# Performance work log

Measured on AMD Instinct MI355X. Metric: run time of the kernel, lower is better.

## Reference

```python
import jax, jax.numpy as jnp
import numpy as np

B, N, D, H = 4, 1024, 1024, 16
DK = D // H
NEG_INF = jnp.finfo(jnp.float32).min


def setup_inputs() -> dict:
    key = jax.random.key(0)
    ks = jax.random.split(key, 6)
    x = jax.random.normal(ks[0], (B, N, D), dtype=jnp.float32)
    # padding mask: True where padded; vary lengths per batch element
    lengths = jnp.array([N, N - 128, N - 256, N - 512], dtype=jnp.int32)
    mask = jnp.arange(N)[None, :] >= lengths[:, None]  # [B, N] bool
    s = (1.0 / np.sqrt(D)).astype(np.float32)  # xavier-ish scale
    Wq = jax.random.normal(ks[1], (D, D), dtype=jnp.float32) * s
    Wk = jax.random.normal(ks[2], (D, D), dtype=jnp.float32) * s
    Wv = jax.random.normal(ks[3], (D, D), dtype=jnp.float32) * s
    Wo = jax.random.normal(ks[4], (D, D), dtype=jnp.float32) * s
    z = jnp.zeros((D,), dtype=jnp.float32)
    return {"x": x, "mask": mask, "Wq": Wq, "bq": z, "Wk": Wk, "bk": z,
            "Wv": Wv, "bv": z, "Wo": Wo, "bo": z}


def reference(x, mask, Wq, bq, Wk, bk, Wv, bv, Wo, bo):
    b, n, d = x.shape
    scale = jnp.asarray(DK, x.dtype) ** -0.5
    # QKV projections (weights stored [out, in] like torch Linear)
    def proj(W, bias):
        y = jnp.einsum('bnd,ed->bne', x, W) + bias
        return y.reshape(b, n, H, DK).transpose(0, 2, 1, 3)  # [B,H,N,Dk]
    q = proj(Wq, bq)
    k = proj(Wk, bk)
    v = proj(Wv, bv)
    energy = jnp.einsum('bhqd,bhkd->bhqk', q, k) * scale  # [B,H,N,N]
    energy = jnp.where(mask[:, None, None, :], NEG_INF, energy)
    weights = jax.nn.softmax(energy, axis=-1)
    attn = jnp.einsum('bhqk,bhkd->bhqd', weights, v)  # [B,H,N,Dk]
    attn = attn.transpose(0, 2, 1, 3).reshape(b, n, d)
    return jnp.einsum('bnd,ed->bne', attn, Wo) + bo
```

## Files before the change

kernel.cpp:

```cpp
#include <hip/hip_runtime.h>

#define DEV __device__ __forceinline__

typedef __attribute__((ext_vector_type(8))) short s16x8;
typedef __attribute__((ext_vector_type(4))) float f32x4;
typedef __attribute__((ext_vector_type(4))) unsigned short u16x4;
typedef __attribute__((ext_vector_type(2))) unsigned int u32x2;

static constexpr int Bb = 4, Nn = 1024, Dd = 1024, Hh = 16, DKk = 64;

DEV unsigned short f2bf(float f) {
    union { float f; unsigned int u; } x; x.f = f;
    unsigned int r = x.u + 0x7FFFu + ((x.u >> 16) & 1u);
    return (unsigned short)(r >> 16);
}

DEV float fexp2(float x) {
#if __has_builtin(__builtin_amdgcn_exp2f)
    return __builtin_amdgcn_exp2f(x);
#else
    return exp2f(x);
#endif
}

DEV void gld16(const void* g, void* l) {
    __builtin_amdgcn_global_load_lds(
        (const __attribute__((address_space(1))) void*)g,
        (__attribute__((address_space(3))) void*)l, 16, 0, 0);
}

DEV void wait_vm4_barrier() {
    __builtin_amdgcn_sched_barrier(0);
    asm volatile("s_waitcnt vmcnt(4)" ::: "memory");
    __builtin_amdgcn_sched_barrier(0);
    __builtin_amdgcn_s_barrier();
}

__global__ __launch_bounds__(256) void cast_k(const float* __restrict__ x,
                                              const float* __restrict__ Wq,
                                              const float* __restrict__ Wk,
                                              const float* __restrict__ Wv,
                                              const float* __restrict__ Wo,
                                              const unsigned int* __restrict__ mraw,
                                              unsigned short* __restrict__ xb,
                                              unsigned short* __restrict__ Wqb,
                                              unsigned short* __restrict__ Wkb,
                                              unsigned short* __restrict__ Wvb,
                                              unsigned short* __restrict__ Wob,
                                              int* __restrict__ lengths) {
    if (blockIdx.x == 4096) {
        __shared__ int is_u8;
        const int tid = threadIdx.x;
        if (tid == 0) is_u8 = 0;
        __syncthreads();
        int nz = 0;
        for (int i = tid; i < 1024; i += 256) nz |= (mraw[i] != 0u) ? 1 : 0;
        if (nz) is_u8 = 1;
        __syncthreads();
        const int wv = tid >> 6, lane = tid & 63;
        int cnt = 0;
        if (is_u8) {
            const unsigned char* b8 = (const unsigned char*)mraw;
            for (int n = lane; n < Nn; n += 64) cnt += (b8[wv * Nn + n] == 0) ? 1 : 0;
        } else {
            for (int n = lane; n < Nn; n += 64) cnt += (mraw[wv * Nn + n] == 0u) ? 1 : 0;
        }
#pragma unroll
        for (int off = 32; off; off >>= 1) cnt += __shfl_xor(cnt, off);
        if (lane == 0) lengths[wv] = cnt;
        return;
    }
    const size_t i = ((size_t)blockIdx.x * 256 + threadIdx.x) * 8;
    const float* src;
    unsigned short* dst;
    size_t off;
    const size_t XE = (size_t)4 * 1024 * 1024, WE = (size_t)1024 * 1024;
    if (i < XE) {
        src = x; dst = xb; off = i;
    } else {
        size_t j = i - XE;
        int w = (int)(j >> 20);
        off = j & (WE - 1);
        src = (w == 0) ? Wq : (w == 1) ? Wk : (w == 2) ? Wv : Wo;
        dst = (w == 0) ? Wqb : (w == 1) ? Wkb : (w == 2) ? Wvb : Wob;
    }
    f32x4 a = *(const f32x4*)(src + off);
    f32x4 b = *(const f32x4*)(src + off + 4);
    s16x8 t;
    t[0] = (short)f2bf(a[0]); t[1] = (short)f2bf(a[1]);
    t[2] = (short)f2bf(a[2]); t[3] = (short)f2bf(a[3]);
    t[4] = (short)f2bf(b[0]); t[5] = (short)f2bf(b[1]);
    t[6] = (short)f2bf(b[2]); t[7] = (short)f2bf(b[3]);
    *(s16x8*)(dst + off) = t;
}

DEV void gemm_kloop(const unsigned short* __restrict__ A,
                    const unsigned short* __restrict__ W,
                    char* lA, char* lB, int bm, int bn,
                    int tid, int kstep0, f32x4 (&acc)[4][4]) {
    const int wv = tid >> 6, lane = tid & 63, g = lane >> 4, lr = lane & 15;
    const int wr = wv >> 1, wc = wv & 1;

    const int rbase = wv * 8 + (lane >> 3);
    const int corig = (lane & 7) ^ (lane >> 3);
    const unsigned short* Asrc = A + (size_t)(bm + rbase) * Dd + corig * 8;
    const unsigned short* Bsrc = W + (size_t)(bn + rbase) * Dd + corig * 8;
    const int ldsb = wv * 1024;
    const int xk = (lr & 7);

    int kstep = kstep0;
    for (int it = 0; it < 16; ++it) {
        const int k0 = kstep * 64;
#pragma unroll
        for (int p = 0; p < 4; ++p) {
            gld16(Asrc + (size_t)(p * 32) * Dd + k0, lA + p * 4096 + ldsb);
            gld16(Bsrc + (size_t)(p * 32) * Dd + k0, lB + p * 4096 + ldsb);
        }
        __syncthreads();
#pragma unroll
        for (int s = 0; s < 2; ++s) {
            s16x8 af[4], bf[4];
#pragma unroll
            for (int m = 0; m < 4; ++m)
                af[m] = *(const s16x8*)(lA + (wr * 64 + m * 16 + lr) * 128 + (((s * 4 + g) ^ xk) << 4));
#pragma unroll
            for (int n = 0; n < 4; ++n)
                bf[n] = *(const s16x8*)(lB + (wc * 64 + n * 16 + lr) * 128 + (((s * 4 + g) ^ xk) << 4));
#pragma unroll
            for (int m = 0; m < 4; ++m)
#pragma unroll
                for (int n = 0; n < 4; ++n)
                    acc[m][n] = __builtin_amdgcn_mfma_f32_16x16x32_bf16(af[m], bf[n], acc[m][n], 0, 0, 0);
        }
        __syncthreads();
        kstep = (kstep + 1) & 15;
    }
}

__global__ __launch_bounds__(256, 4) void gemm_qkv_k(const unsigned short* __restrict__ xb,
                                                     const unsigned short* __restrict__ Wqb,
                                                     const unsigned short* __restrict__ Wkb,
                                                     const unsigned short* __restrict__ Wvb,
                                                     const float* __restrict__ bq,
                                                     const float* __restrict__ bk,
                                                     const float* __restrict__ bv,
                                                     const int* __restrict__ lengths,
                                                     unsigned short* __restrict__ Qo,
                                                     unsigned short* __restrict__ Ko,
                                                     unsigned short* __restrict__ Vo) {
    __shared__ __align__(16) char lA[128 * 64 * 2];
    __shared__ __align__(16) char lB[128 * 64 * 2];
    const int z = blockIdx.z;
    const int bm = blockIdx.x * 128, bn = blockIdx.y * 128;
    if (z != 0 && (bm & 1023) >= lengths[bm >> 10]) return;

    const unsigned short* W = (z == 0) ? Wqb : (z == 1) ? Wkb : Wvb;
    const float* bias = (z == 0) ? bq : (z == 1) ? bk : bv;

    const int tid = threadIdx.x;
    const int wv = tid >> 6, lane = tid & 63, g = lane >> 4, lr = lane & 15;
    const int wr = wv >> 1, wc = wv & 1;
    const int kstep0 = (blockIdx.x * 5 + blockIdx.y * 3 + z * 7) & 15;

    f32x4 acc[4][4];
#pragma unroll
    for (int m = 0; m < 4; ++m)
#pragma unroll
        for (int n = 0; n < 4; ++n) acc[m][n] = (f32x4){0.f, 0.f, 0.f, 0.f};

    gemm_kloop(xb, W, lA, lB, bm, bn, tid, kstep0, acc);

    const int row0 = bm + wr * 64 + g * 4;
    if (z == 0) {
        const float qs = 0.125f * 1.44269504f;
#pragma unroll
        for (int m = 0; m < 4; ++m)
#pragma unroll
            for (int n = 0; n < 4; ++n) {
                const int col = bn + wc * 64 + n * 16 + lr;
                const float bv_ = bias[col];
#pragma unroll
                for (int r = 0; r < 4; ++r)
                    Qo[(size_t)(row0 + m * 16 + r) * Dd + col] = f2bf((acc[m][n][r] + bv_) * qs);
            }
    } else if (z == 1) {
#pragma unroll
        for (int m = 0; m < 4; ++m)
#pragma unroll
            for (int n = 0; n < 4; ++n) {
                const int col = bn + wc * 64 + n * 16 + lr;
                const int h = col >> 6, dk = col & 63;
                const float bv_ = bias[col];
#pragma unroll
                for (int r = 0; r < 4; ++r) {
                    const int rowg = row0 + m * 16 + r;
                    const int b_ = rowg >> 10, tok = rowg & 1023;
                    size_t idx = ((size_t)(b_ * Hh + h) * Nn + tok) * DKk +
                                 (((dk >> 3) ^ (tok & 7)) << 3) + (dk & 7);
                    Ko[idx] = f2bf(acc[m][n][r] + bv_);
                }
            }
    } else {
#pragma unroll
        for (int m = 0; m < 4; ++m)
#pragma unroll
            for (int n = 0; n < 4; ++n) {
                const int col = bn + wc * 64 + n * 16 + lr;
                const int h = col >> 6, dk = col & 63;
                const float bv_ = bias[col];
                const int rowg = row0 + m * 16;
                const int b_ = rowg >> 10, tok = rowg & 1023;
                u16x4 t;
#pragma unroll
                for (int r = 0; r < 4; ++r) t[r] = f2bf(acc[m][n][r] + bv_);
                size_t idx = ((size_t)(b_ * Hh + h) * DKk + dk) * Nn + (tok & ~63) +
                             ((((tok >> 3) & 7) ^ (dk & 7)) << 3) + (tok & 7);
                *(u16x4*)(Vo + idx) = t;
            }
    }
}

__global__ __launch_bounds__(256, 4) void gemm_out_k(const unsigned short* __restrict__ Ab,
                                                     const unsigned short* __restrict__ Wob,
                                                     const float* __restrict__ bo,
                                                     float* __restrict__ out) {
    __shared__ __align__(16) char lA[128 * 64 * 2];
    __shared__ __align__(16) char lB[128 * 64 * 2];
    const int tid = threadIdx.x;
    const int wv = tid >> 6, lane = tid & 63, g = lane >> 4, lr = lane & 15;
    const int wr = wv >> 1, wc = wv & 1;
    const int bm = blockIdx.x * 128, bn = blockIdx.y * 128;
    const int kstep0 = (blockIdx.x * 5 + blockIdx.y * 3) & 15;

    f32x4 acc[4][4];
#pragma unroll
    for (int m = 0; m < 4; ++m)
#pragma unroll
        for (int n = 0; n < 4; ++n) acc[m][n] = (f32x4){0.f, 0.f, 0.f, 0.f};

    gemm_kloop(Ab, Wob, lA, lB, bm, bn, tid, kstep0, acc);

    const int row0 = bm + wr * 64 + g * 4;
#pragma unroll
    for (int m = 0; m < 4; ++m)
#pragma unroll
        for (int n = 0; n < 4; ++n) {
            const int col = bn + wc * 64 + n * 16 + lr;
            const float bv_ = bo[col];
#pragma unroll
            for (int r = 0; r < 4; ++r)
                out[(size_t)(row0 + m * 16 + r) * Dd + col] = acc[m][n][r] + bv_;
        }
}

__global__ __launch_bounds__(256) void attn_k(const unsigned short* __restrict__ Q,
                                              const unsigned short* __restrict__ Kg,
                                              const unsigned short* __restrict__ Vtg,
                                              const int* __restrict__ lengths,
                                              unsigned short* __restrict__ O) {
    const int tid = threadIdx.x;
    const int wv = tid >> 6, lane = tid & 63, g = lane >> 4, lr = lane & 15;
    const int bid = blockIdx.x;
    const int qt = bid & 15, h = (bid >> 4) & 15, b = bid >> 8;
    const int len = lengths[b];
    const int nt = (len + 63) >> 6;

    __shared__ __align__(16) char Ks[2 * 64 * 128];
    __shared__ __align__(16) char Vs[2 * 64 * 128];
    __shared__ __align__(16) char Ps[4][16 * 128];

    s16x8 qf[2];
    {
        const int qrow = b * Nn + qt * 64 + wv * 16 + lr;
        const unsigned short* qp = Q + (size_t)qrow * Dd + h * DKk + g * 8;
        qf[0] = *(const s16x8*)qp;
        qf[1] = *(const s16x8*)(qp + 32);
    }

    float m_run = 0.f, l_run = 0.f;
    f32x4 oacc[4];
#pragma unroll
    for (int dt = 0; dt < 4; ++dt) oacc[dt] = (f32x4){0.f, 0.f, 0.f, 0.f};

    const int s0 = wv * 64 + lane;
    const int r0 = s0 >> 3, c0 = s0 & 7;
    const int r1 = r0 + 32;
    const unsigned short* Kbase = Kg + (size_t)(b * Hh + h) * Nn * DKk;
    const unsigned short* Vbase = Vtg + (size_t)(b * Hh + h) * DKk * Nn;

    const int xk16 = (lr & 7) << 4;
    const int shsrc = (lane & 48) | (g * 4);

    gld16(Kbase + (size_t)r0 * DKk + c0 * 8, Ks + wv * 1024);
    gld16(Kbase + (size_t)r1 * DKk + c0 * 8, Ks + wv * 1024 + 4096);
    gld16(Vbase + (size_t)r0 * Nn + c0 * 8, Vs + wv * 1024);
    gld16(Vbase + (size_t)r1 * Nn + c0 * 8, Vs + wv * 1024 + 4096);

    int cur = 0;
    for (int kt = 0; kt < nt; ++kt) {
        const int kb = kt * 64;
        {
            const int kb2 = (kt + 1 < nt) ? kb + 64 : 0;
            const int nb = (cur ^ 1) * 8192;
            gld16(Kbase + (size_t)(kb2 + r0) * DKk + c0 * 8, Ks + nb + wv * 1024);
            gld16(Kbase + (size_t)(kb2 + r1) * DKk + c0 * 8, Ks + nb + wv * 1024 + 4096);
            gld16(Vbase + (size_t)r0 * Nn + kb2 + c0 * 8, Vs + nb + wv * 1024);
            gld16(Vbase + (size_t)r1 * Nn + kb2 + c0 * 8, Vs + nb + wv * 1024 + 4096);
        }
        wait_vm4_barrier();

        const char* ks_ = Ks + cur * 8192;
        const char* vs_ = Vs + cur * 8192;

        const float nm = -m_run;
        f32x4 sfr[4];
        __builtin_amdgcn_s_setprio(1);
#pragma unroll
        for (int ct = 0; ct < 4; ++ct) {
            f32x4 c = (f32x4){nm, nm, nm, nm};
#pragma unroll
            for (int s = 0; s < 2; ++s) {
                s16x8 kf = *(const s16x8*)(ks_ + (ct * 16 + lr) * 128 + ((((s * 4 + g) << 4)) ^ xk16));
                c = __builtin_amdgcn_mfma_f32_16x16x32_bf16(kf, qf[s], c, 0, 0, 0);
            }
            sfr[ct] = c;
        }
        __builtin_amdgcn_s_setprio(0);

        float mx = -INFINITY;
        if (kb + 64 <= len) {
#pragma unroll
            for (int ct = 0; ct < 4; ++ct)
#pragma unroll
                for (int r = 0; r < 4; ++r) mx = fmaxf(mx, sfr[ct][r]);
        } else {
#pragma unroll
            for (int ct = 0; ct < 4; ++ct) {
                const int kb4 = kb + ct * 16 + g * 4;
#pragma unroll
                for (int r = 0; r < 4; ++r) {
                    const float s_ = (kb4 + r < len) ? sfr[ct][r] : -INFINITY;
                    sfr[ct][r] = s_;
                    mx = fmaxf(mx, s_);
                }
            }
        }
        mx = fmaxf(mx, __shfl_xor(mx, 16));
        mx = fmaxf(mx, __shfl_xor(mx, 32));

        float ls = 0.f;
        if (__any(mx > 8.f)) {
            const float dm = fmaxf(mx, 0.f);
            const float alpha = fexp2(-dm);
            m_run += dm;
            l_run *= alpha;
            float ao[4];
#pragma unroll
            for (int r = 0; r < 4; ++r) ao[r] = __shfl(alpha, shsrc + r);
#pragma unroll
            for (int dt = 0; dt < 4; ++dt)
#pragma unroll
                for (int r = 0; r < 4; ++r) oacc[dt][r] *= ao[r];
#pragma unroll
            for (int ct = 0; ct < 4; ++ct)
#pragma unroll
                for (int r = 0; r < 4; ++r) {
                    const float p = fexp2(sfr[ct][r] - dm);
                    sfr[ct][r] = p;
                    ls += p;
                }
        } else {
#pragma unroll
            for (int ct = 0; ct < 4; ++ct)
#pragma unroll
                for (int r = 0; r < 4; ++r) {
                    const float p = fexp2(sfr[ct][r]);
                    sfr[ct][r] = p;
                    ls += p;
                }
        }
        ls += __shfl_xor(ls, 16);
        ls += __shfl_xor(ls, 32);
        l_run += ls;

#pragma unroll
        for (int ct = 0; ct < 4; ++ct) {
            unsigned int w0, w1;
            asm("v_cvt_pk_bf16_f32 %0, %1, %2" : "=v"(w0) : "v"(sfr[ct][0]), "v"(sfr[ct][1]));
            asm("v_cvt_pk_bf16_f32 %0, %1, %2" : "=v"(w1) : "v"(sfr[ct][2]), "v"(sfr[ct][3]));
            u32x2 wp; wp[0] = w0; wp[1] = w1;
            *(u32x2*)(Ps[wv] + lr * 128 + ((ct * 32 + g * 8) ^ xk16)) = wp;
        }

        __builtin_amdgcn_s_setprio(1);
#pragma unroll
        for (int s = 0; s < 2; ++s) {
            s16x8 pf = *(const s16x8*)(Ps[wv] + lr * 128 + ((((s * 4 + g) << 4)) ^ xk16));
#pragma unroll
            for (int dt = 0; dt < 4; ++dt) {
                s16x8 vf = *(const s16x8*)(vs_ + (dt * 16 + lr) * 128 + ((((s * 4 + g) << 4)) ^ xk16));
                oacc[dt] = __builtin_amdgcn_mfma_f32_16x16x32_bf16(pf, vf, oacc[dt], 0, 0, 0);
            }
        }
        __builtin_amdgcn_s_setprio(0);
        __builtin_amdgcn_s_barrier();
        cur ^= 1;
    }

    float lo[4];
#pragma unroll
    for (int r = 0; r < 4; ++r) lo[r] = __shfl(l_run, shsrc + r);
#pragma unroll
    for (int dt = 0; dt < 4; ++dt) {
        const int col = h * DKk + dt * 16 + lr;
#pragma unroll
        for (int r = 0; r < 4; ++r) {
            const int row = qt * 64 + wv * 16 + g * 4 + r;
            float v = oacc[dt][r] / lo[r];
            O[(size_t)(b * Nn + row) * Dd + col] = f2bf(v);
        }
    }
}

extern "C" void kernel_launch(void* const* d_in, const int* in_sizes, int n_in,
                              void* d_out, int out_size, void* d_ws, size_t ws_size,
                              hipStream_t stream) {
    const float* x  = (const float*)d_in[0];
    const unsigned int* mraw = (const unsigned int*)d_in[1];
    const float* Wq = (const float*)d_in[2];
    const float* bq = (const float*)d_in[3];
    const float* Wk = (const float*)d_in[4];
    const float* bk = (const float*)d_in[5];
    const float* Wv = (const float*)d_in[6];
    const float* bv = (const float*)d_in[7];
    const float* Wo = (const float*)d_in[8];
    const float* bo = (const float*)d_in[9];

    char* ws = (char*)d_ws;
    int* lengths        = (int*)ws;                      ws += 1 << 16;
    unsigned short* xb  = (unsigned short*)ws;           ws += (size_t)Bb * Nn * Dd * 2;
    unsigned short* Wqb = (unsigned short*)ws;           ws += (size_t)Dd * Dd * 2;
    unsigned short* Wkb = (unsigned short*)ws;           ws += (size_t)Dd * Dd * 2;
    unsigned short* Wvb = (unsigned short*)ws;           ws += (size_t)Dd * Dd * 2;
    unsigned short* Wob = (unsigned short*)ws;           ws += (size_t)Dd * Dd * 2;
    unsigned short* Qb  = (unsigned short*)ws;           ws += (size_t)Bb * Nn * Dd * 2;
    unsigned short* Kg  = (unsigned short*)ws;           ws += (size_t)Bb * Nn * Dd * 2;
    unsigned short* Vtg = (unsigned short*)ws;           ws += (size_t)Bb * Nn * Dd * 2;
    unsigned short* Ab  = (unsigned short*)ws;

    cast_k<<<4097, 256, 0, stream>>>(x, Wq, Wk, Wv, Wo, mraw,
                                     xb, Wqb, Wkb, Wvb, Wob, lengths);

    dim3 qkv_grid(Bb * Nn / 128, Dd / 128, 3);
    gemm_qkv_k<<<qkv_grid, 256, 0, stream>>>(xb, Wqb, Wkb, Wvb, bq, bk, bv, lengths,
                                             Qb, Kg, Vtg);

    attn_k<<<Bb * Hh * (Nn / 64), 256, 0, stream>>>(Qb, Kg, Vtg, lengths, Ab);

    dim3 out_grid(Bb * Nn / 128, Dd / 128);
    gemm_out_k<<<out_grid, 256, 0, stream>>>(Ab, Wob, bo, (float*)d_out);
}
```

Baseline: 91.38 us.

## Widen attention blocks to 128 queries and shrink output GEMM row tile to 64

The attention kernel now runs 512-thread blocks that cover 128 query rows, so each K/V tile loaded into LDS is shared by eight waves instead of four. Each thread issues one K and one V load per stage, and the wait count drops to match. The output projection GEMM gets a custom 64x128 tile loop instead of the shared 128x128 k-loop, doubling the block count to fill more CUs. The trade-off is fewer, heavier attention blocks and a simpler, non-pipelined GEMM loop with two syncthreads per k-step.

```diff
diff --git a/kernel.cpp b/kernel.cpp
--- a/kernel.cpp
+++ b/kernel.cpp
@@ -29,9 +29,9 @@
         (__attribute__((address_space(3))) void*)l, 16, 0, 0);
 }
 
-DEV void wait_vm4_barrier() {
+DEV void wait_vm2_barrier() {
     __builtin_amdgcn_sched_barrier(0);
-    asm volatile("s_waitcnt vmcnt(4)" ::: "memory");
+    asm volatile("s_waitcnt vmcnt(2)" ::: "memory");
     __builtin_amdgcn_sched_barrier(0);
     __builtin_amdgcn_s_barrier();
 }
@@ -224,25 +224,59 @@
                                                      const unsigned short* __restrict__ Wob,
                                                      const float* __restrict__ bo,
                                                      float* __restrict__ out) {
-    __shared__ __align__(16) char lA[128 * 64 * 2];
+    __shared__ __align__(16) char lA[64 * 64 * 2];
     __shared__ __align__(16) char lB[128 * 64 * 2];
     const int tid = threadIdx.x;
     const int wv = tid >> 6, lane = tid & 63, g = lane >> 4, lr = lane & 15;
     const int wr = wv >> 1, wc = wv & 1;
-    const int bm = blockIdx.x * 128, bn = blockIdx.y * 128;
+    const int bm = blockIdx.x * 64, bn = blockIdx.y * 128;
     const int kstep0 = (blockIdx.x * 5 + blockIdx.y * 3) & 15;
 
-    f32x4 acc[4][4];
-#pragma unroll
-    for (int m = 0; m < 4; ++m)
+    f32x4 acc[2][4];
+#pragma unroll
+    for (int m = 0; m < 2; ++m)
 #pragma unroll
         for (int n = 0; n < 4; ++n) acc[m][n] = (f32x4){0.f, 0.f, 0.f, 0.f};
 
-    gemm_kloop(Ab, Wob, lA, lB, bm, bn, tid, kstep0, acc);
-
-    const int row0 = bm + wr * 64 + g * 4;
-#pragma unroll
-    for (int m = 0; m < 4; ++m)
+    const int rbase = wv * 8 + (lane >> 3);
+    const int corig = (lane & 7) ^ (lane >> 3);
+    const unsigned short* Asrc = Ab + (size_t)(bm + rbase) * Dd + corig * 8;
+    const unsigned short* Bsrc = Wob + (size_t)(bn + rbase) * Dd + corig * 8;
+    const int ldsb = wv * 1024;
+    const int xk = (lr & 7);
+
+    int kstep = kstep0;
+    for (int it = 0; it < 16; ++it) {
+        const int k0 = kstep * 64;
+#pragma unroll
+        for (int p = 0; p < 2; ++p)
+            gld16(Asrc + (size_t)(p * 32) * Dd + k0, lA + p * 4096 + ldsb);
+#pragma unroll
+        for (int p = 0; p < 4; ++p)
+            gld16(Bsrc + (size_t)(p * 32) * Dd + k0, lB + p * 4096 + ldsb);
+        __syncthreads();
+#pragma unroll
+        for (int s = 0; s < 2; ++s) {
+            s16x8 af[2], bf[4];
+#pragma unroll
+            for (int m = 0; m < 2; ++m)
+                af[m] = *(const s16x8*)(lA + (wr * 32 + m * 16 + lr) * 128 + (((s * 4 + g) ^ xk) << 4));
+#pragma unroll
+            for (int n = 0; n < 4; ++n)
+                bf[n] = *(const s16x8*)(lB + (wc * 64 + n * 16 + lr) * 128 + (((s * 4 + g) ^ xk) << 4));
+#pragma unroll
+            for (int m = 0; m < 2; ++m)
+#pragma unroll
+                for (int n = 0; n < 4; ++n)
+                    acc[m][n] = __builtin_amdgcn_mfma_f32_16x16x32_bf16(af[m], bf[n], acc[m][n], 0, 0, 0);
+        }
+        __syncthreads();
+        kstep = (kstep + 1) & 15;
+    }
+
+    const int row0 = bm + wr * 32 + g * 4;
+#pragma unroll
+    for (int m = 0; m < 2; ++m)
 #pragma unroll
         for (int n = 0; n < 4; ++n) {
             const int col = bn + wc * 64 + n * 16 + lr;
@@ -253,7 +287,7 @@
         }
 }
 
-__global__ __launch_bounds__(256) void attn_k(const unsigned short* __restrict__ Q,
+__global__ __launch_bounds__(512) void attn_k(const unsigned short* __restrict__ Q,
                                               const unsigned short* __restrict__ Kg,
                                               const unsigned short* __restrict__ Vtg,
                                               const int* __restrict__ lengths,
@@ -261,17 +295,17 @@
     const int tid = threadIdx.x;
     const int wv = tid >> 6, lane = tid & 63, g = lane >> 4, lr = lane & 15;
     const int bid = blockIdx.x;
-    const int qt = bid & 15, h = (bid >> 4) & 15, b = bid >> 8;
+    const int qt = bid & 7, h = (bid >> 3) & 15, b = bid >> 7;
     const int len = lengths[b];
     const int nt = (len + 63) >> 6;
 
     __shared__ __align__(16) char Ks[2 * 64 * 128];
     __shared__ __align__(16) char Vs[2 * 64 * 128];
-    __shared__ __align__(16) char Ps[4][16 * 128];
+    __shared__ __align__(16) char Ps[8][16 * 128];
 
     s16x8 qf[2];
     {
-        const int qrow = b * Nn + qt * 64 + wv * 16 + lr;
+        const int qrow = b * Nn + qt * 128 + wv * 16 + lr;
         const unsigned short* qp = Q + (size_t)qrow * Dd + h * DKk + g * 8;
         qf[0] = *(const s16x8*)qp;
         qf[1] = *(const s16x8*)(qp + 32);
@@ -282,19 +316,15 @@
 #pragma unroll
     for (int dt = 0; dt < 4; ++dt) oacc[dt] = (f32x4){0.f, 0.f, 0.f, 0.f};
 
-    const int s0 = wv * 64 + lane;
-    const int r0 = s0 >> 3, c0 = s0 & 7;
-    const int r1 = r0 + 32;
+    const int r0 = tid >> 3, c0 = tid & 7;
     const unsigned short* Kbase = Kg + (size_t)(b * Hh + h) * Nn * DKk;
     const unsigned short* Vbase = Vtg + (size_t)(b * Hh + h) * DKk * Nn;
 
     const int xk16 = (lr & 7) << 4;
     const int shsrc = (lane & 48) | (g * 4);
 
-    gld16(Kbase + (size_t)r0 * DKk + c0 * 8, Ks + wv * 1024);
-    gld16(Kbase + (size_t)r1 * DKk + c0 * 8, Ks + wv * 1024 + 4096);
-    gld16(Vbase + (size_t)r0 * Nn + c0 * 8, Vs + wv * 1024);
-    gld16(Vbase + (size_t)r1 * Nn + c0 * 8, Vs + wv * 1024 + 4096);
+    gld16(Kbase + (size_t)r0 * DKk + c0 * 8, Ks + tid * 16);
+    gld16(Vbase + (size_t)r0 * Nn + c0 * 8, Vs + tid * 16);
 
     int cur = 0;
     for (int kt = 0; kt < nt; ++kt) {
@@ -302,12 +332,10 @@
         {
             const int kb2 = (kt + 1 < nt) ? kb + 64 : 0;
             const int nb = (cur ^ 1) * 8192;
-            gld16(Kbase + (size_t)(kb2 + r0) * DKk + c0 * 8, Ks + nb + wv * 1024);
-            gld16(Kbase + (size_t)(kb2 + r1) * DKk + c0 * 8, Ks + nb + wv * 1024 + 4096);
-            gld16(Vbase + (size_t)r0 * Nn + kb2 + c0 * 8, Vs + nb + wv * 1024);
-            gld16(Vbase + (size_t)r1 * Nn + kb2 + c0 * 8, Vs + nb + wv * 1024 + 4096);
-        }
-        wait_vm4_barrier();
+            gld16(Kbase + (size_t)(kb2 + r0) * DKk + c0 * 8, Ks + nb + tid * 16);
+            gld16(Vbase + (size_t)r0 * Nn + kb2 + c0 * 8, Vs + nb + tid * 16);
+        }
+        wait_vm2_barrier();
 
         const char* ks_ = Ks + cur * 8192;
         const char* vs_ = Vs + cur * 8192;
@@ -415,7 +443,7 @@
         const int col = h * DKk + dt * 16 + lr;
 #pragma unroll
         for (int r = 0; r < 4; ++r) {
-            const int row = qt * 64 + wv * 16 + g * 4 + r;
+            const int row = qt * 128 + wv * 16 + g * 4 + r;
             float v = oacc[dt][r] / lo[r];
             O[(size_t)(b * Nn + row) * Dd + col] = f2bf(v);
         }
@@ -455,8 +483,8 @@
     gemm_qkv_k<<<qkv_grid, 256, 0, stream>>>(xb, Wqb, Wkb, Wvb, bq, bk, bv, lengths,
                                              Qb, Kg, Vtg);
 
-    attn_k<<<Bb * Hh * (Nn / 64), 256, 0, stream>>>(Qb, Kg, Vtg, lengths, Ab);
-
-    dim3 out_grid(Bb * Nn / 128, Dd / 128);
+    attn_k<<<Bb * Hh * (Nn / 128), 512, 0, stream>>>(Qb, Kg, Vtg, lengths, Ab);
+
+    dim3 out_grid(Bb * Nn / 64, Dd / 128);
     gemm_out_k<<<out_grid, 256, 0, stream>>>(Ab, Wob, bo, (float*)d_out);
 }
```

Result: faster. 89.23 us, median of 2 (-2.3%).
